# Kernel optimization log

Measured on AMD Instinct MI355X. Metric: run time of the kernel, lower is better.

Reference implementation:

```python
import jax, jax.numpy as jnp
import numpy as np

THRESH = 0.3  # ternary threshold on |W|/mean(|W|)

def ternary_quantize(W):
    # scale = mean(|W|) clamped; q in {-1,0,+1} * scale
    scale = jnp.maximum(jnp.mean(jnp.abs(W)), 1e-8)
    ws = W / scale
    q = jnp.where(ws > THRESH, 1.0, jnp.where(ws < -THRESH, -1.0, 0.0))
    return q * scale

def quantize_activations(y):
    # per-token (last-dim) max-abs int8-style fake quant
    m = jnp.maximum(jnp.max(jnp.abs(y), axis=-1, keepdims=True), 1e-5)
    scale = 127.0 / m
    return jnp.round(jnp.clip(y * scale, -127.0, 127.0)) / scale

def setup_inputs() -> dict:
    key = jax.random.key(0)
    k1, k2, k3, k4, k5 = jax.random.split(key, 5)
    N, D_IN, D_OUT = 16384, 2048, 2048
    x = jax.random.normal(k1, (N, D_IN), dtype=jnp.float32)
    W = jax.random.normal(k2, (D_OUT, D_IN), dtype=jnp.float32) * 0.02
    b = jax.random.normal(k3, (D_OUT,), dtype=jnp.float32) * 0.02
    We = jax.random.normal(k4, (D_OUT, D_IN), dtype=jnp.float32) * 0.02
    be = jax.random.normal(k5, (D_OUT,), dtype=jnp.float32) * 0.02
    return {"x": x, "W": W, "b": b, "We": We, "be": be}

def reference(x, W, b, We, be):
    chain = jax.nn.relu(x @ ternary_quantize(W).T + b)  # [N, D_OUT]
    encoded = x @ We.T + be                              # [N, D_OUT]
    return quantize_activations(chain + encoded)
```

## Files before the change

### kernel.cpp

```cpp
#include <hip/hip_runtime.h>
#include <hip/hip_bf16.h>
#include <math.h>

typedef __bf16 bf16;
typedef __bf16 bf16x8 __attribute__((ext_vector_type(8)));
typedef float  f32x4  __attribute__((ext_vector_type(4)));
typedef unsigned int u32;

#define NROWS 16384
#define KDIM  2048
#define NCOLS 2048

#define OFF_XBF   0
#define OFF_Q     67108864
#define OFF_EBF   75497472
#define OFF_PART  83886080
#define OFF_SCALE 83894272

__device__ __forceinline__ void gload16(const bf16* g, bf16* l) {
    __builtin_amdgcn_global_load_lds(
        (const __attribute__((address_space(1))) u32*)g,
        (__attribute__((address_space(3))) u32*)l,
        16, 0, 0);
}

__global__ void k_rowsum_absW(const float* __restrict__ W, float* __restrict__ partials) {
    int row = blockIdx.x;
    int t = threadIdx.x;
    const float4* wr = (const float4*)(W + (size_t)row * KDIM);
    float4 a = wr[t * 2];
    float4 b = wr[t * 2 + 1];
    float s = fabsf(a.x) + fabsf(a.y) + fabsf(a.z) + fabsf(a.w)
            + fabsf(b.x) + fabsf(b.y) + fabsf(b.z) + fabsf(b.w);
    __shared__ float red[256];
    red[t] = s; __syncthreads();
    for (int off = 128; off > 0; off >>= 1) {
        if (t < off) red[t] += red[t + off];
        __syncthreads();
    }
    if (t == 0) partials[row] = red[0];
}

__global__ void k_scale(const float* __restrict__ partials, float* __restrict__ scale) {
    int t = threadIdx.x;
    double s = 0.0;
    for (int i = t; i < 2048; i += 256) s += (double)partials[i];
    __shared__ double red[256];
    red[t] = s; __syncthreads();
    for (int off = 128; off > 0; off >>= 1) {
        if (t < off) red[t] += red[t + off];
        __syncthreads();
    }
    if (t == 0) {
        float m = (float)(red[0] / 4194304.0);
        scale[0] = fmaxf(m, 1e-8f);
    }
}

__global__ void k_quant(const float* __restrict__ W, const float* __restrict__ We,
                        const float* __restrict__ scale_p,
                        bf16* __restrict__ q, bf16* __restrict__ ebf) {
    float scale = scale_p[0];
    size_t base = ((size_t)blockIdx.x * 256 + threadIdx.x) * 8;
    float4 w0 = *(const float4*)(W + base);
    float4 w1 = *(const float4*)(W + base + 4);
    float4 e0 = *(const float4*)(We + base);
    float4 e1 = *(const float4*)(We + base + 4);
    float wv[8] = {w0.x, w0.y, w0.z, w0.w, w1.x, w1.y, w1.z, w1.w};
    float ev[8] = {e0.x, e0.y, e0.z, e0.w, e1.x, e1.y, e1.z, e1.w};
    bf16x8 qv, bv;
#pragma unroll
    for (int i = 0; i < 8; i++) {
        float ws = wv[i] / scale;
        float qq = ws > 0.3f ? 1.0f : (ws < -0.3f ? -1.0f : 0.0f);
        qv[i] = (bf16)qq;
        bv[i] = (bf16)ev[i];
    }
    *(bf16x8*)(q + base)   = qv;
    *(bf16x8*)(ebf + base) = bv;
}

__global__ void k_cvt_x(const float* __restrict__ x, bf16* __restrict__ xbf) {
    size_t base = ((size_t)blockIdx.x * 256 + threadIdx.x) * 8;
    float4 a = *(const float4*)(x + base);
    float4 c = *(const float4*)(x + base + 4);
    float v[8] = {a.x, a.y, a.z, a.w, c.x, c.y, c.z, c.w};
    bf16x8 o;
#pragma unroll
    for (int i = 0; i < 8; i++) o[i] = (bf16)v[i];
    *(bf16x8*)(xbf + base) = o;
}

#define BM 128
#define BN 128
#define BK 64

__global__ __launch_bounds__(512)
void k_gemm_dual(const bf16* __restrict__ X, const bf16* __restrict__ Q,
                 const bf16* __restrict__ E,
                 const float* __restrict__ b, const float* __restrict__ be,
                 const float* __restrict__ scale_p, float* __restrict__ Y)
{
    __shared__ bf16 lA [BM * BK];
    __shared__ bf16 lB1[BN * BK];
    __shared__ bf16 lB2[BN * BK];

    int t    = threadIdx.x;
    int lane = t & 63;
    int w    = t >> 6;
    int wr   = w >> 2;
    int wc   = w & 3;

    int bCol = blockIdx.x;
    int bRow = blockIdx.y;

    const bf16* gA  = X + (size_t)(bRow * BM) * KDIM;
    const bf16* gB1 = Q + (size_t)(bCol * BN) * KDIM;
    const bf16* gB2 = E + (size_t)(bCol * BN) * KDIM;

    int row0 = t >> 3;
    int colsw = ((t & 7) * 8) ^ ((row0 & 7) << 3);

    f32x4 acc1[4][2], acc2[4][2];
#pragma unroll
    for (int m = 0; m < 4; m++)
#pragma unroll
        for (int n = 0; n < 2; n++) {
            acc1[m][n] = (f32x4){0.f, 0.f, 0.f, 0.f};
            acc2[m][n] = (f32x4){0.f, 0.f, 0.f, 0.f};
        }

    int lrow = lane & 15;
    int lk   = lane >> 4;

    for (int k0 = 0; k0 < KDIM; k0 += BK) {
#pragma unroll
        for (int it = 0; it < 2; ++it) {
            int row = row0 + it * 64;
            int off = (it * 512 + t) * 8;
            gload16(gA  + (size_t)row * KDIM + k0 + colsw, &lA [off]);
            gload16(gB1 + (size_t)row * KDIM + k0 + colsw, &lB1[off]);
            gload16(gB2 + (size_t)row * KDIM + k0 + colsw, &lB2[off]);
        }
        __syncthreads();

#pragma unroll
        for (int kk = 0; kk < 2; kk++) {
            int ko = kk * 32 + lk * 8;
            bf16x8 af[4], bq[2], beo[2];
#pragma unroll
            for (int m = 0; m < 4; m++) {
                int ar = wr * 64 + m * 16 + lrow;
                af[m] = *(const bf16x8*)&lA[ar * BK + (ko ^ ((ar & 7) << 3))];
            }
#pragma unroll
            for (int n = 0; n < 2; n++) {
                int br = wc * 32 + n * 16 + lrow;
                int sc = ko ^ ((br & 7) << 3);
                bq [n] = *(const bf16x8*)&lB1[br * BK + sc];
                beo[n] = *(const bf16x8*)&lB2[br * BK + sc];
            }
#pragma unroll
            for (int m = 0; m < 4; m++)
#pragma unroll
                for (int n = 0; n < 2; n++) {
                    acc1[m][n] = __builtin_amdgcn_mfma_f32_16x16x32_bf16(af[m], bq [n], acc1[m][n], 0, 0, 0);
                    acc2[m][n] = __builtin_amdgcn_mfma_f32_16x16x32_bf16(af[m], beo[n], acc2[m][n], 0, 0, 0);
                }
        }
        __syncthreads();
    }

    float scale = scale_p[0];
#pragma unroll
    for (int m = 0; m < 4; m++) {
        int gr0 = bRow * BM + wr * 64 + m * 16 + (lane >> 4) * 4;
#pragma unroll
        for (int n = 0; n < 2; n++) {
            int gc = bCol * BN + wc * 32 + n * 16 + (lane & 15);
            float bj  = b[gc];
            float bej = be[gc];
#pragma unroll
            for (int v = 0; v < 4; v++) {
                float chain = fmaxf(acc1[m][n][v] * scale + bj, 0.0f);
                float y = chain + acc2[m][n][v] + bej;
                Y[(size_t)(gr0 + v) * NCOLS + gc] = y;
            }
        }
    }
}

__global__ void k_quant_rows(float* __restrict__ Y) {
    int row = blockIdx.x;
    int t = threadIdx.x;
    float4* yv = (float4*)(Y + (size_t)row * NCOLS);
    float4 a = yv[t];
    float4 c = yv[t + 256];
    float mx = fmaxf(fmaxf(fmaxf(fabsf(a.x), fabsf(a.y)), fmaxf(fabsf(a.z), fabsf(a.w))),
                     fmaxf(fmaxf(fabsf(c.x), fabsf(c.y)), fmaxf(fabsf(c.z), fabsf(c.w))));
    __shared__ float red[256];
    red[t] = mx; __syncthreads();
    for (int off = 128; off > 0; off >>= 1) {
        if (t < off) red[t] = fmaxf(red[t], red[t + off]);
        __syncthreads();
    }
    float m = fmaxf(red[0], 1e-5f);
    float qs = 127.0f / m;
    float4 oa, oc;
    oa.x = rintf(fminf(fmaxf(a.x * qs, -127.f), 127.f)) / qs;
    oa.y = rintf(fminf(fmaxf(a.y * qs, -127.f), 127.f)) / qs;
    oa.z = rintf(fminf(fmaxf(a.z * qs, -127.f), 127.f)) / qs;
    oa.w = rintf(fminf(fmaxf(a.w * qs, -127.f), 127.f)) / qs;
    oc.x = rintf(fminf(fmaxf(c.x * qs, -127.f), 127.f)) / qs;
    oc.y = rintf(fminf(fmaxf(c.y * qs, -127.f), 127.f)) / qs;
    oc.z = rintf(fminf(fmaxf(c.z * qs, -127.f), 127.f)) / qs;
    oc.w = rintf(fminf(fmaxf(c.w * qs, -127.f), 127.f)) / qs;
    yv[t] = oa;
    yv[t + 256] = oc;
}

extern "C" void kernel_launch(void* const* d_in, const int* in_sizes, int n_in,
                              void* d_out, int out_size, void* d_ws, size_t ws_size,
                              hipStream_t stream) {
    const float* x  = (const float*)d_in[0];
    const float* W  = (const float*)d_in[1];
    const float* b  = (const float*)d_in[2];
    const float* We = (const float*)d_in[3];
    const float* be = (const float*)d_in[4];
    float* out = (float*)d_out;

    char* ws = (char*)d_ws;
    bf16*  xbf      = (bf16*)(ws + OFF_XBF);
    bf16*  q        = (bf16*)(ws + OFF_Q);
    bf16*  ebf      = (bf16*)(ws + OFF_EBF);
    float* partials = (float*)(ws + OFF_PART);
    float* scale    = (float*)(ws + OFF_SCALE);

    k_rowsum_absW<<<2048, 256, 0, stream>>>(W, partials);
    k_scale<<<1, 256, 0, stream>>>(partials, scale);
    k_quant<<<2048, 256, 0, stream>>>(W, We, scale, q, ebf);
    k_cvt_x<<<16384, 256, 0, stream>>>(x, xbf);

    dim3 g(NCOLS / BN, NROWS / BM);
    k_gemm_dual<<<g, 512, 0, stream>>>(xbf, q, ebf, b, be, scale, out);

    k_quant_rows<<<NROWS, 256, 0, stream>>>(out);
}
```

Baseline: 317.7 us.

## Triple-buffer dual GEMM LDS loads with manual waitcnt pipeline and tile swizzle

Replaces the single-buffered load-sync-compute loop with a three-stage LDS ring. Global-to-LDS loads for step T+2 are issued while step T computes, using explicit vmcnt waits and raw barriers in place of full syncthreads. It also remaps block IDs so that blocks landing on the same XCD share column tiles, and raises wave priority around the MFMA bursts. LDS use per block grows to about 144KB, which caps occupancy at one block per CU, and the correctness of the hand-counted waitcnt values depends on how the compiler orders the loads.

```diff
diff --git a/kernel.cpp b/kernel.cpp
--- a/kernel.cpp
+++ b/kernel.cpp
@@ -22,6 +22,12 @@
         (const __attribute__((address_space(1))) u32*)g,
         (__attribute__((address_space(3))) u32*)l,
         16, 0, 0);
+}
+
+__device__ __forceinline__ void BAR() {
+    asm volatile("" ::: "memory");
+    __builtin_amdgcn_s_barrier();
+    asm volatile("" ::: "memory");
 }
 
 __global__ void k_rowsum_absW(const float* __restrict__ W, float* __restrict__ partials) {
@@ -94,6 +100,8 @@
 #define BM 128
 #define BN 128
 #define BK 64
+#define KSTEPS (KDIM / BK)
+#define BUFE (BM * BK + 2 * BN * BK)
 
 __global__ __launch_bounds__(512)
 void k_gemm_dual(const bf16* __restrict__ X, const bf16* __restrict__ Q,
@@ -101,9 +109,7 @@
                  const float* __restrict__ b, const float* __restrict__ be,
                  const float* __restrict__ scale_p, float* __restrict__ Y)
 {
-    __shared__ bf16 lA [BM * BK];
-    __shared__ bf16 lB1[BN * BK];
-    __shared__ bf16 lB2[BN * BK];
+    __shared__ bf16 lds[3][BUFE];
 
     int t    = threadIdx.x;
     int lane = t & 63;
@@ -111,8 +117,10 @@
     int wr   = w >> 2;
     int wc   = w & 3;
 
-    int bCol = blockIdx.x;
-    int bRow = blockIdx.y;
+    int id   = blockIdx.x;
+    int swz  = (id & 7) * 256 + (id >> 3);
+    int bRow = swz >> 4;
+    int bCol = swz & 15;
 
     const bf16* gA  = X + (size_t)(bRow * BM) * KDIM;
     const bf16* gB1 = Q + (size_t)(bCol * BN) * KDIM;
@@ -133,17 +141,23 @@
     int lrow = lane & 15;
     int lk   = lane >> 4;
 
-    for (int k0 = 0; k0 < KDIM; k0 += BK) {
-#pragma unroll
-        for (int it = 0; it < 2; ++it) {
-            int row = row0 + it * 64;
-            int off = (it * 512 + t) * 8;
-            gload16(gA  + (size_t)row * KDIM + k0 + colsw, &lA [off]);
-            gload16(gB1 + (size_t)row * KDIM + k0 + colsw, &lB1[off]);
-            gload16(gB2 + (size_t)row * KDIM + k0 + colsw, &lB2[off]);
-        }
-        __syncthreads();
-
+    auto STAGE = [&](int buf, int ks) {
+        bf16* LA  = &lds[buf][0];
+        bf16* LB1 = &lds[buf][BM * BK];
+        bf16* LB2 = &lds[buf][BM * BK + BN * BK];
+        size_t kof = (size_t)ks * BK + colsw;
+        gload16(gA  + (size_t)row0 * KDIM + kof,        &LA [t * 8]);
+        gload16(gA  + (size_t)(row0 + 64) * KDIM + kof, &LA [(512 + t) * 8]);
+        gload16(gB1 + (size_t)row0 * KDIM + kof,        &LB1[t * 8]);
+        gload16(gB1 + (size_t)(row0 + 64) * KDIM + kof, &LB1[(512 + t) * 8]);
+        gload16(gB2 + (size_t)row0 * KDIM + kof,        &LB2[t * 8]);
+        gload16(gB2 + (size_t)(row0 + 64) * KDIM + kof, &LB2[(512 + t) * 8]);
+    };
+
+    auto COMPUTE = [&](int buf) {
+        const bf16* LA  = &lds[buf][0];
+        const bf16* LB1 = &lds[buf][BM * BK];
+        const bf16* LB2 = &lds[buf][BM * BK + BN * BK];
 #pragma unroll
         for (int kk = 0; kk < 2; kk++) {
             int ko = kk * 32 + lk * 8;
@@ -151,15 +165,16 @@
 #pragma unroll
             for (int m = 0; m < 4; m++) {
                 int ar = wr * 64 + m * 16 + lrow;
-                af[m] = *(const bf16x8*)&lA[ar * BK + (ko ^ ((ar & 7) << 3))];
+                af[m] = *(const bf16x8*)&LA[ar * BK + (ko ^ ((ar & 7) << 3))];
             }
 #pragma unroll
             for (int n = 0; n < 2; n++) {
                 int br = wc * 32 + n * 16 + lrow;
                 int sc = ko ^ ((br & 7) << 3);
-                bq [n] = *(const bf16x8*)&lB1[br * BK + sc];
-                beo[n] = *(const bf16x8*)&lB2[br * BK + sc];
+                bq [n] = *(const bf16x8*)&LB1[br * BK + sc];
+                beo[n] = *(const bf16x8*)&LB2[br * BK + sc];
             }
+            __builtin_amdgcn_s_setprio(1);
 #pragma unroll
             for (int m = 0; m < 4; m++)
 #pragma unroll
@@ -167,9 +182,30 @@
                     acc1[m][n] = __builtin_amdgcn_mfma_f32_16x16x32_bf16(af[m], bq [n], acc1[m][n], 0, 0, 0);
                     acc2[m][n] = __builtin_amdgcn_mfma_f32_16x16x32_bf16(af[m], beo[n], acc2[m][n], 0, 0, 0);
                 }
+            __builtin_amdgcn_s_setprio(0);
         }
-        __syncthreads();
-    }
+    };
+
+    STAGE(0, 0);
+    STAGE(1, 1);
+
+#pragma unroll 1
+    for (int T = 0; T < KSTEPS - 2; ++T) {
+        STAGE((T + 2) % 3, T + 2);
+        asm volatile("s_waitcnt vmcnt(12)" ::: "memory");
+        BAR();
+        COMPUTE(T % 3);
+        asm volatile("s_waitcnt lgkmcnt(0)" ::: "memory");
+        BAR();
+    }
+    asm volatile("s_waitcnt vmcnt(6)" ::: "memory");
+    BAR();
+    COMPUTE((KSTEPS - 2) % 3);
+    asm volatile("s_waitcnt lgkmcnt(0)" ::: "memory");
+    BAR();
+    asm volatile("s_waitcnt vmcnt(0)" ::: "memory");
+    BAR();
+    COMPUTE((KSTEPS - 1) % 3);
 
     float scale = scale_p[0];
 #pragma unroll
@@ -241,8 +277,7 @@
     k_quant<<<2048, 256, 0, stream>>>(W, We, scale, q, ebf);
     k_cvt_x<<<16384, 256, 0, stream>>>(x, xbf);
 
-    dim3 g(NCOLS / BN, NROWS / BM);
-    k_gemm_dual<<<g, 512, 0, stream>>>(xbf, q, ebf, b, be, scale, out);
+    k_gemm_dual<<<(NROWS / BM) * (NCOLS / BN), 512, 0, stream>>>(xbf, q, ebf, b, be, scale, out);
 
     k_quant_rows<<<NROWS, 256, 0, stream>>>(out);
 }
```

After: 375.5 us. 18.2% more time.
